# Performance work log

Measured on AMD Instinct MI355X. Metric: run time of the kernel, lower is better.

## Reference

```python
import jax, jax.numpy as jnp
import numpy as np

NUM_TYPES = 4
IN_DIM = 128
HID_DIM = 256
OUT_DIM = 128
NUM_NODES = 100000


def setup_inputs() -> dict:
    key = jax.random.key(0)
    k_x, k_t, k_w1, k_b1, k_w2, k_b2 = jax.random.split(key, 6)
    raw_features = jax.random.normal(k_x, (NUM_NODES, IN_DIM), dtype=jnp.float32)
    node_type = jax.random.randint(k_t, (NUM_NODES,), 0, NUM_TYPES, dtype=jnp.int64)
    # stacked per-type MLP params (Kaiming-ish scale like torch Linear defaults)
    W1 = jax.random.uniform(k_w1, (NUM_TYPES, IN_DIM, HID_DIM), dtype=jnp.float32,
                            minval=-1.0, maxval=1.0) / np.sqrt(IN_DIM)
    b1 = jax.random.uniform(k_b1, (NUM_TYPES, HID_DIM), dtype=jnp.float32,
                            minval=-1.0, maxval=1.0) / np.sqrt(IN_DIM)
    W2 = jax.random.uniform(k_w2, (NUM_TYPES, HID_DIM, OUT_DIM), dtype=jnp.float32,
                            minval=-1.0, maxval=1.0) / np.sqrt(HID_DIM)
    b2 = jax.random.uniform(k_b2, (NUM_TYPES, OUT_DIM), dtype=jnp.float32,
                            minval=-1.0, maxval=1.0) / np.sqrt(HID_DIM)
    return {"raw_features": raw_features, "node_type": node_type,
            "W1": W1, "b1": b1, "W2": W2, "b2": b2}


def reference(raw_features, node_type, W1, b1, W2, b2):
    # Run every expert on every node (num_types is tiny), then select per node.
    # h: [types, nodes, hidden]
    h = jax.nn.relu(jnp.einsum('ni,tih->tnh', raw_features, W1) + b1[:, None, :])
    # out_all: [types, nodes, out]
    out_all = jnp.einsum('tnh,tho->tno', h, W2) + b2[:, None, :]
    # select expert output matching each node's type -> [nodes, out]
    encoded = out_all[node_type, jnp.arange(raw_features.shape[0])]
    return encoded
```

## Files before the change

kernel.cpp:

```cpp
#include <hip/hip_runtime.h>
#include <hip/hip_bf16.h>

typedef float f32x4 __attribute__((ext_vector_type(4)));
typedef short short8 __attribute__((ext_vector_type(8)));

#define NTYPES 4


static __device__ __forceinline__ unsigned short f2bf(float f) {
  union { float f; unsigned int u; } v; v.f = f;
  unsigned int u = v.u;
  unsigned int r = u + 0x7FFFu + ((u >> 16) & 1u);
  return (unsigned short)(r >> 16);
}

static __device__ __forceinline__ unsigned int pkbf(float a, float b) {
  __hip_bfloat162 h = __float22bfloat162_rn(make_float2(a, b));
  union { __hip_bfloat162 h; unsigned int u; } v; v.h = h;
  return v.u;
}

#define LBAR() do { \
  __builtin_amdgcn_sched_barrier(0); \
  asm volatile("s_waitcnt lgkmcnt(0)" ::: "memory"); \
  __builtin_amdgcn_s_barrier(); \
  __builtin_amdgcn_sched_barrier(0); } while (0)

static __device__ __forceinline__ void prep_tile(int role, int tid,
    const float* __restrict__ W1, const float* __restrict__ W2,
    unsigned short* __restrict__ W1T, unsigned short* __restrict__ W2T,
    unsigned short (*sp)[72]) {
  const int bb = role & 31;
  const int tt = bb >> 3, ti = bb & 7;
  const float* src; unsigned short* dst; int scols, tr, tc;
  if (role < 32) { src = W1 + tt * 32768; dst = W1T + tt * 32768; scols = 256; tr = ti >> 2; tc = ti & 3; }
  else           { src = W2 + tt * 32768; dst = W2T + tt * 32768; scols = 128; tr = ti >> 1; tc = ti & 1; }
  const int srows = 32768 / scols;
  const int r0 = tid >> 4, cw = (tid & 15) << 2;
  #pragma unroll
  for (int i = 0; i < 4; ++i) {
    int r = tr * 64 + i * 16 + r0;
    float4 v = *(const float4*)(src + r * scols + tc * 64 + cw);
    sp[i * 16 + r0][cw + 0] = f2bf(v.x);
    sp[i * 16 + r0][cw + 1] = f2bf(v.y);
    sp[i * 16 + r0][cw + 2] = f2bf(v.z);
    sp[i * 16 + r0][cw + 3] = f2bf(v.w);
  }
  __syncthreads();
  #pragma unroll
  for (int i = 0; i < 4; ++i) {
    int orow = i * 16 + r0;
    ushort4 u;
    u.x = sp[cw + 0][orow];
    u.y = sp[cw + 1][orow];
    u.z = sp[cw + 2][orow];
    u.w = sp[cw + 3][orow];
    *(ushort4*)(dst + (tc * 64 + orow) * srows + tr * 64 + cw) = u;
  }
}

static __device__ __forceinline__ void mlp_body(
    int t, int lb, int nblk, int g0, int g1, int tid,
    const float* __restrict__ X, const int* __restrict__ perm,
    const unsigned short* __restrict__ W1T, const unsigned short* __restrict__ W2T,
    const float* __restrict__ B1, const float* __restrict__ B2,
    float* __restrict__ OUT, float* __restrict__ dump,
    unsigned char* x_lds, unsigned char* h_lds, int (*s_rid)[64]) {
  const int l  = tid & 63, w = tid >> 6;
  const int lo = l & 15,  hi = l >> 4;
  const int nt2 = g1 - g0 - lb;
  if (nt2 <= 0) return;
  const int cnt = (nt2 + nblk - 1) / nblk;

  const int rg = tid >> 5;
  const int c4 = (tid & 31) * 4;

  if (tid < 64) s_rid[0][tid] = perm[(g0 + lb) * 64 + tid];
  __syncthreads();
  float4 xv[8];
  #pragma unroll
  for (int p = 0; p < 8; ++p) {
    int rd = s_rid[0][p * 8 + rg];
    xv[p] = make_float4(0.f, 0.f, 0.f, 0.f);
    if (rd >= 0) xv[p] = *(const float4*)(X + (size_t)rd * 128 + c4);
  }

  const unsigned short* w1t = W1T + (t << 15);
  const unsigned short* w2t = W2T + (t << 15);
  short8 a1[4][4];
  #pragma unroll
  for (int ks = 0; ks < 4; ++ks)
    #pragma unroll
    for (int m = 0; m < 4; ++m)
      a1[ks][m] = *(const short8*)(w1t + (w * 64 + m * 16 + lo) * 128 + ks * 32 + hi * 8);
  short8 a2[8][2];
  #pragma unroll
  for (int ks = 0; ks < 8; ++ks)
    #pragma unroll
    for (int mo = 0; mo < 2; ++mo)
      a2[ks][mo] = *(const short8*)(w2t + (w * 32 + mo * 16 + lo) * 256 + ks * 32 + hi * 8);
  f32x4 bb1[4], bb2[2];
  #pragma unroll
  for (int m = 0; m < 4; ++m)
    bb1[m] = *(const f32x4*)(B1 + t * 256 + w * 64 + m * 16 + hi * 4);
  #pragma unroll
  for (int mo = 0; mo < 2; ++mo)
    bb2[mo] = *(const f32x4*)(B2 + t * 128 + w * 32 + mo * 16 + hi * 4);

  for (int j = 0; j < cnt; ++j) {
    const int g = g0 + lb + j * nblk;
    const bool hn = (j + 1 < cnt);
    const int cur = j & 1, nxt = cur ^ 1;
    unsigned char* xb = x_lds + (j & 1) * 16384;

    #pragma unroll
    for (int p = 0; p < 8; ++p) {
      int row = p * 8 + rg;
      uint2 u;
      u.x = pkbf(xv[p].x, xv[p].y);
      u.y = pkbf(xv[p].z, xv[p].w);
      int byte = (row * 256 + c4 * 2) ^ ((row & 7) << 4);
      *(uint2*)(xb + byte) = u;
    }
    LBAR();

    if (hn && tid < 64) s_rid[nxt][tid] = perm[(g + nblk) * 64 + tid];

    f32x4 acc[4][4];
    #pragma unroll
    for (int m = 0; m < 4; ++m)
      #pragma unroll
      for (int n2 = 0; n2 < 4; ++n2) acc[m][n2] = (f32x4){0.f, 0.f, 0.f, 0.f};
    #pragma unroll
    for (int ks = 0; ks < 4; ++ks) {
      short8 b[4];
      #pragma unroll
      for (int n2 = 0; n2 < 4; ++n2) {
        int row = n2 * 16 + lo;
        int byte = (row * 256 + ks * 64 + hi * 16) ^ ((row & 7) << 4);
        b[n2] = *(const short8*)(xb + byte);
      }
      #pragma unroll
      for (int m = 0; m < 4; ++m)
        #pragma unroll
        for (int n2 = 0; n2 < 4; ++n2)
          acc[m][n2] = __builtin_amdgcn_mfma_f32_16x16x32_bf16(a1[ks][m], b[n2], acc[m][n2], 0, 0, 0);
    }

    #pragma unroll
    for (int m = 0; m < 4; ++m) {
      const int hw2 = w * 128 + m * 32 + hi * 8;
      #pragma unroll
      for (int n2 = 0; n2 < 4; ++n2) {
        int node = n2 * 16 + lo;
        uint2 hu;
        hu.x = pkbf(fmaxf(acc[m][n2][0] + bb1[m][0], 0.f),
                    fmaxf(acc[m][n2][1] + bb1[m][1], 0.f));
        hu.y = pkbf(fmaxf(acc[m][n2][2] + bb1[m][2], 0.f),
                    fmaxf(acc[m][n2][3] + bb1[m][3], 0.f));
        int byte = (node * 512 + hw2) ^ ((node & 7) << 4);
        *(uint2*)(h_lds + byte) = hu;
      }
    }
    LBAR();

    float4 nv[8];
    #pragma unroll
    for (int p = 0; p < 8; ++p) nv[p] = make_float4(0.f, 0.f, 0.f, 0.f);
    if (hn) {
      #pragma unroll
      for (int p = 0; p < 8; ++p) {
        int rd = s_rid[nxt][p * 8 + rg];
        if (rd >= 0) nv[p] = *(const float4*)(X + (size_t)rd * 128 + c4);
      }
    }

    f32x4 acc2[2][4];
    #pragma unroll
    for (int mo = 0; mo < 2; ++mo)
      #pragma unroll
      for (int n2 = 0; n2 < 4; ++n2) acc2[mo][n2] = (f32x4){0.f, 0.f, 0.f, 0.f};
    #pragma unroll
    for (int ks = 0; ks < 8; ++ks) {
      short8 b[4];
      #pragma unroll
      for (int n2 = 0; n2 < 4; ++n2) {
        int node = n2 * 16 + lo;
        int byte = (node * 512 + ks * 64 + hi * 16) ^ ((node & 7) << 4);
        b[n2] = *(const short8*)(h_lds + byte);
      }
      #pragma unroll
      for (int mo = 0; mo < 2; ++mo)
        #pragma unroll
        for (int n2 = 0; n2 < 4; ++n2)
          acc2[mo][n2] = __builtin_amdgcn_mfma_f32_16x16x32_bf16(a2[ks][mo], b[n2], acc2[mo][n2], 0, 0, 0);
    }
    __syncthreads();

    #pragma unroll
    for (int mo = 0; mo < 2; ++mo) {
      const int oc = w * 32 + mo * 16 + hi * 4;
      #pragma unroll
      for (int n2 = 0; n2 < 4; ++n2) {
        int node = n2 * 16 + lo;
        f32x4 o = acc2[mo][n2];
        o[0] += bb2[mo][0]; o[1] += bb2[mo][1];
        o[2] += bb2[mo][2]; o[3] += bb2[mo][3];
        int byte = (node * 512 + oc * 4) ^ ((node & 7) << 4);
        *(f32x4*)(h_lds + byte) = o;
      }
    }
    LBAR();

    #pragma unroll
    for (int p = 0; p < 8; ++p) {
      int row = p * 8 + rg;
      int rd = s_rid[cur][row];
      f32x4 v = *(const f32x4*)(h_lds + ((row * 512 + c4 * 4) ^ ((row & 7) << 4)));
      float* dst = (rd >= 0) ? (OUT + (size_t)rd * 128 + c4) : (dump + c4);
      *(f32x4*)dst = v;
    }

    #pragma unroll
    for (int p = 0; p < 8; ++p) xv[p] = nv[p];
  }
}

__global__ __launch_bounds__(256) void k_hp(
    const float* __restrict__ W1, const float* __restrict__ W2,
    unsigned short* __restrict__ W1T, unsigned short* __restrict__ W2T,
    const int* __restrict__ NT, int n, int* __restrict__ cnts) {
  __shared__ unsigned short sp[64][72];
  __shared__ int lc[NTYPES];
  const int tid = threadIdx.x;
  if (blockIdx.x < 64) {
    prep_tile(blockIdx.x, tid, W1, W2, W1T, W2T, sp);
  } else {
    int hb = blockIdx.x - 64;
    if (tid < NTYPES) lc[tid] = 0;
    __syncthreads();
    int i = hb * 256 + tid;
    if (i < n) atomicAdd(&lc[NT[i]], 1);
    __syncthreads();
    if (tid < NTYPES) cnts[hb * NTYPES + tid] = lc[tid];
  }
}

__global__ __launch_bounds__(256) void k_scatter2(
    const int* __restrict__ NT, int n, const int* __restrict__ cnts, int nbH,
    int* __restrict__ perm, int* __restrict__ bases) {
  __shared__ int s_tot[NTYPES], s_pre[NTYPES], lc[NTYPES];
  const int tid = threadIdx.x;
  const int bid = blockIdx.x;
  const int l = tid & 63, w = tid >> 6;
  {
    int tot = 0, pre = 0;
    for (int b = l; b < nbH; b += 64) {
      int c = cnts[b * NTYPES + w];
      tot += c;
      pre += (b < bid) ? c : 0;
    }
    #pragma unroll
    for (int off = 32; off; off >>= 1) {
      tot += __shfl_down(tot, off);
      pre += __shfl_down(pre, off);
    }
    if (l == 0) { s_tot[w] = tot; s_pre[w] = pre; }
  }
  __syncthreads();
  int sb[NTYPES + 1];
  sb[0] = 0;
  #pragma unroll
  for (int tau = 0; tau < NTYPES; ++tau)
    sb[tau + 1] = sb[tau] + ((s_tot[tau] + 63) & ~63);
  if (bid == 0 && tid <= NTYPES) bases[tid] = sb[tid];
  if (tid < NTYPES) lc[tid] = 0;
  __syncthreads();
  int i = bid * 256 + tid;
  if (i < n) {
    int tt = NT[i];
    int r = atomicAdd(&lc[tt], 1);
    perm[sb[tt] + s_pre[tt] + r] = i;
  }
  if (bid < NTYPES) {
    for (int p = sb[bid] + s_tot[bid] + tid; p < sb[bid + 1]; p += 256)
      perm[p] = -1;
  }
}

__global__ __launch_bounds__(256, 1) void k_mlpw_fb(
    const float* __restrict__ X, const int* __restrict__ perm,
    const int* __restrict__ bases,
    const unsigned short* __restrict__ W1T, const unsigned short* __restrict__ W2T,
    const float* __restrict__ B1, const float* __restrict__ B2,
    float* __restrict__ OUT, float* __restrict__ dump) {
  __shared__ __align__(16) unsigned char x_lds[2 * 16384];
  __shared__ __align__(16) unsigned char h_lds[32768];
  __shared__ int s_rid[2][64];
  const int t = blockIdx.x >> 7, lb = blockIdx.x & 127;
  mlp_body(t, lb, 128, bases[t] >> 6, bases[t + 1] >> 6, threadIdx.x,
           X, perm, W1T, W2T, B1, B2, OUT, dump, x_lds, h_lds, s_rid);
}

extern "C" void kernel_launch(void* const* d_in, const int* in_sizes, int n_in,
                              void* d_out, int out_size, void* d_ws, size_t ws_size,
                              hipStream_t stream) {
  const float* X  = (const float*)d_in[0];
  const int*   NT = (const int*)d_in[1];
  const float* W1 = (const float*)d_in[2];
  const float* B1 = (const float*)d_in[3];
  const float* W2 = (const float*)d_in[4];
  const float* B2 = (const float*)d_in[5];
  float* OUT = (float*)d_out;
  int n = in_sizes[1];

  char* ws = (char*)d_ws;
  float* dump = (float*)(ws + 512);
  int* bases = (int*)(ws + 2048);
  int* cnts = (int*)(ws + 4096);
  int* perm = (int*)(ws + 16384);
  unsigned short* W1T = (unsigned short*)(ws + 524288);
  unsigned short* W2T = (unsigned short*)(ws + 786432);

  const int nbH = (n + 255) / 256;
  k_hp<<<64 + nbH, 256, 0, stream>>>(W1, W2, W1T, W2T, NT, n, cnts);
  k_scatter2<<<nbH, 256, 0, stream>>>(NT, n, cnts, nbH, perm, bases);
  k_mlpw_fb<<<512, 256, 0, stream>>>(X, perm, bases, W1T, W2T, B1, B2, OUT, dump);
}
```

Baseline: 51.28 us.

## Software-pipeline MLP layers across tiles with double-buffered hidden LDS and direct stores

Rewrites the grouped MLP kernel so that layer 1 of tile j and layer 2 of tile j-1 run in the same iteration, using double-buffered hidden activations in LDS. This drops to one barrier per iteration. Output goes straight from the accumulators to global memory instead of being staged through LDS, and per-row ids are read into registers rather than shared memory. The grid is halved from 512 to 256 blocks, one per CU with 64 blocks per type, so each block handles more tiles. The changes aim to cut barrier stalls and LDS traffic, at the cost of uncoalesced 16-byte output stores, repeated perm loads, and 96KB of LDS per block.

```diff
diff --git a/kernel.cpp b/kernel.cpp
--- a/kernel.cpp
+++ b/kernel.cpp
@@ -59,31 +59,28 @@
   }
 }
 
-static __device__ __forceinline__ void mlp_body(
-    int t, int lb, int nblk, int g0, int g1, int tid,
+__global__ __launch_bounds__(256, 1) void k_mlpn(
     const float* __restrict__ X, const int* __restrict__ perm,
+    const int* __restrict__ bases,
     const unsigned short* __restrict__ W1T, const unsigned short* __restrict__ W2T,
     const float* __restrict__ B1, const float* __restrict__ B2,
-    float* __restrict__ OUT, float* __restrict__ dump,
-    unsigned char* x_lds, unsigned char* h_lds, int (*s_rid)[64]) {
+    float* __restrict__ OUT) {
+  __shared__ __align__(16) unsigned char x_lds[2 * 16384];
+  __shared__ __align__(16) unsigned char h_lds[2 * 32768];
+
+  const int tid = threadIdx.x;
+  const int t  = blockIdx.x >> 6;
+  const int lb = blockIdx.x & 63;
+  const int g0 = bases[t] >> 6;
+  const int g1 = bases[t + 1] >> 6;
+  const int nt2 = g1 - g0 - lb;
+  if (nt2 <= 0) return;
+  const int cnt = (nt2 + 63) >> 6;
+
   const int l  = tid & 63, w = tid >> 6;
   const int lo = l & 15,  hi = l >> 4;
-  const int nt2 = g1 - g0 - lb;
-  if (nt2 <= 0) return;
-  const int cnt = (nt2 + nblk - 1) / nblk;
-
   const int rg = tid >> 5;
   const int c4 = (tid & 31) * 4;
-
-  if (tid < 64) s_rid[0][tid] = perm[(g0 + lb) * 64 + tid];
-  __syncthreads();
-  float4 xv[8];
-  #pragma unroll
-  for (int p = 0; p < 8; ++p) {
-    int rd = s_rid[0][p * 8 + rg];
-    xv[p] = make_float4(0.f, 0.f, 0.f, 0.f);
-    if (rd >= 0) xv[p] = *(const float4*)(X + (size_t)rd * 128 + c4);
-  }
 
   const unsigned short* w1t = W1T + (t << 15);
   const unsigned short* w2t = W2T + (t << 15);
@@ -107,122 +104,136 @@
   for (int mo = 0; mo < 2; ++mo)
     bb2[mo] = *(const f32x4*)(B2 + t * 128 + w * 32 + mo * 16 + hi * 4);
 
-  for (int j = 0; j < cnt; ++j) {
-    const int g = g0 + lb + j * nblk;
-    const bool hn = (j + 1 < cnt);
-    const int cur = j & 1, nxt = cur ^ 1;
-    unsigned char* xb = x_lds + (j & 1) * 16384;
-
+  int rid_n[8];
+  float4 xv_n[8];
+  {
+    const int gg = (g0 + lb) * 64;
+    #pragma unroll
+    for (int p = 0; p < 8; ++p) rid_n[p] = perm[gg + p * 8 + rg];
+    #pragma unroll
+    for (int p = 0; p < 8; ++p) {
+      xv_n[p] = make_float4(0.f, 0.f, 0.f, 0.f);
+      if (rid_n[p] >= 0) xv_n[p] = *(const float4*)(X + (size_t)rid_n[p] * 128 + c4);
+    }
     #pragma unroll
     for (int p = 0; p < 8; ++p) {
       int row = p * 8 + rg;
       uint2 u;
-      u.x = pkbf(xv[p].x, xv[p].y);
-      u.y = pkbf(xv[p].z, xv[p].w);
-      int byte = (row * 256 + c4 * 2) ^ ((row & 7) << 4);
-      *(uint2*)(xb + byte) = u;
-    }
+      u.x = pkbf(xv_n[p].x, xv_n[p].y);
+      u.y = pkbf(xv_n[p].z, xv_n[p].w);
+      *(uint2*)(x_lds + ((row * 256 + c4 * 2) ^ ((row & 7) << 4))) = u;
+    }
+  }
+
+  for (int j = 0; j <= cnt; ++j) {
+    const int g = g0 + lb + j * 64;
+    const bool hn = (j + 1 < cnt);
+    const bool h1 = (j < cnt);
+    unsigned char* xb = x_lds + (j & 1) * 16384;
+    unsigned char* hb = h_lds + (j & 1) * 32768;
+    unsigned char* hp = h_lds + ((j & 1) ^ 1) * 32768;
+
     LBAR();
 
-    if (hn && tid < 64) s_rid[nxt][tid] = perm[(g + nblk) * 64 + tid];
-
-    f32x4 acc[4][4];
-    #pragma unroll
-    for (int m = 0; m < 4; ++m)
-      #pragma unroll
-      for (int n2 = 0; n2 < 4; ++n2) acc[m][n2] = (f32x4){0.f, 0.f, 0.f, 0.f};
-    #pragma unroll
-    for (int ks = 0; ks < 4; ++ks) {
-      short8 b[4];
-      #pragma unroll
-      for (int n2 = 0; n2 < 4; ++n2) {
-        int row = n2 * 16 + lo;
-        int byte = (row * 256 + ks * 64 + hi * 16) ^ ((row & 7) << 4);
-        b[n2] = *(const short8*)(xb + byte);
-      }
+    if (hn) {
+      const int gg = (g + 64) * 64;
+      #pragma unroll
+      for (int p = 0; p < 8; ++p) rid_n[p] = perm[gg + p * 8 + rg];
+      #pragma unroll
+      for (int p = 0; p < 8; ++p) {
+        xv_n[p] = make_float4(0.f, 0.f, 0.f, 0.f);
+        if (rid_n[p] >= 0) xv_n[p] = *(const float4*)(X + (size_t)rid_n[p] * 128 + c4);
+      }
+    }
+
+    if (h1) {
+      f32x4 acc[4][4];
       #pragma unroll
       for (int m = 0; m < 4; ++m)
         #pragma unroll
-        for (int n2 = 0; n2 < 4; ++n2)
-          acc[m][n2] = __builtin_amdgcn_mfma_f32_16x16x32_bf16(a1[ks][m], b[n2], acc[m][n2], 0, 0, 0);
-    }
-
-    #pragma unroll
-    for (int m = 0; m < 4; ++m) {
-      const int hw2 = w * 128 + m * 32 + hi * 8;
-      #pragma unroll
-      for (int n2 = 0; n2 < 4; ++n2) {
-        int node = n2 * 16 + lo;
-        uint2 hu;
-        hu.x = pkbf(fmaxf(acc[m][n2][0] + bb1[m][0], 0.f),
-                    fmaxf(acc[m][n2][1] + bb1[m][1], 0.f));
-        hu.y = pkbf(fmaxf(acc[m][n2][2] + bb1[m][2], 0.f),
-                    fmaxf(acc[m][n2][3] + bb1[m][3], 0.f));
-        int byte = (node * 512 + hw2) ^ ((node & 7) << 4);
-        *(uint2*)(h_lds + byte) = hu;
-      }
-    }
-    LBAR();
-
-    float4 nv[8];
-    #pragma unroll
-    for (int p = 0; p < 8; ++p) nv[p] = make_float4(0.f, 0.f, 0.f, 0.f);
+        for (int n2 = 0; n2 < 4; ++n2) acc[m][n2] = (f32x4){0.f, 0.f, 0.f, 0.f};
+      #pragma unroll
+      for (int ks = 0; ks < 4; ++ks) {
+        short8 b[4];
+        #pragma unroll
+        for (int n2 = 0; n2 < 4; ++n2) {
+          int row = n2 * 16 + lo;
+          int byte = (row * 256 + ks * 64 + hi * 16) ^ ((row & 7) << 4);
+          b[n2] = *(const short8*)(xb + byte);
+        }
+        #pragma unroll
+        for (int m = 0; m < 4; ++m)
+          #pragma unroll
+          for (int n2 = 0; n2 < 4; ++n2)
+            acc[m][n2] = __builtin_amdgcn_mfma_f32_16x16x32_bf16(a1[ks][m], b[n2], acc[m][n2], 0, 0, 0);
+      }
+      #pragma unroll
+      for (int m = 0; m < 4; ++m) {
+        const int hw2 = w * 128 + m * 32 + hi * 8;
+        #pragma unroll
+        for (int n2 = 0; n2 < 4; ++n2) {
+          int node = n2 * 16 + lo;
+          uint2 hu;
+          hu.x = pkbf(fmaxf(acc[m][n2][0] + bb1[m][0], 0.f),
+                      fmaxf(acc[m][n2][1] + bb1[m][1], 0.f));
+          hu.y = pkbf(fmaxf(acc[m][n2][2] + bb1[m][2], 0.f),
+                      fmaxf(acc[m][n2][3] + bb1[m][3], 0.f));
+          int byte = (node * 512 + hw2) ^ ((node & 7) << 4);
+          *(uint2*)(hb + byte) = hu;
+        }
+      }
+    }
+
+    if (j > 0) {
+      f32x4 acc2[2][4];
+      #pragma unroll
+      for (int mo = 0; mo < 2; ++mo)
+        #pragma unroll
+        for (int n2 = 0; n2 < 4; ++n2) acc2[mo][n2] = (f32x4){0.f, 0.f, 0.f, 0.f};
+      #pragma unroll
+      for (int ks = 0; ks < 8; ++ks) {
+        short8 b[4];
+        #pragma unroll
+        for (int n2 = 0; n2 < 4; ++n2) {
+          int node = n2 * 16 + lo;
+          int byte = (node * 512 + ks * 64 + hi * 16) ^ ((node & 7) << 4);
+          b[n2] = *(const short8*)(hp + byte);
+        }
+        #pragma unroll
+        for (int mo = 0; mo < 2; ++mo)
+          #pragma unroll
+          for (int n2 = 0; n2 < 4; ++n2)
+            acc2[mo][n2] = __builtin_amdgcn_mfma_f32_16x16x32_bf16(a2[ks][mo], b[n2], acc2[mo][n2], 0, 0, 0);
+      }
+      const int gp = (g - 64) * 64;
+      #pragma unroll
+      for (int mo = 0; mo < 2; ++mo) {
+        const int oc = w * 32 + mo * 16 + hi * 4;
+        #pragma unroll
+        for (int n2 = 0; n2 < 4; ++n2) {
+          int row = n2 * 16 + lo;
+          int rd = perm[gp + row];
+          if (rd >= 0) {
+            f32x4 o = acc2[mo][n2];
+            o[0] += bb2[mo][0]; o[1] += bb2[mo][1];
+            o[2] += bb2[mo][2]; o[3] += bb2[mo][3];
+            *(f32x4*)(OUT + (size_t)rd * 128 + oc) = o;
+          }
+        }
+      }
+    }
+
     if (hn) {
+      unsigned char* xn = x_lds + ((j & 1) ^ 1) * 16384;
       #pragma unroll
       for (int p = 0; p < 8; ++p) {
-        int rd = s_rid[nxt][p * 8 + rg];
-        if (rd >= 0) nv[p] = *(const float4*)(X + (size_t)rd * 128 + c4);
-      }
-    }
-
-    f32x4 acc2[2][4];
-    #pragma unroll
-    for (int mo = 0; mo < 2; ++mo)
-      #pragma unroll
-      for (int n2 = 0; n2 < 4; ++n2) acc2[mo][n2] = (f32x4){0.f, 0.f, 0.f, 0.f};
-    #pragma unroll
-    for (int ks = 0; ks < 8; ++ks) {
-      short8 b[4];
-      #pragma unroll
-      for (int n2 = 0; n2 < 4; ++n2) {
-        int node = n2 * 16 + lo;
-        int byte = (node * 512 + ks * 64 + hi * 16) ^ ((node & 7) << 4);
-        b[n2] = *(const short8*)(h_lds + byte);
-      }
-      #pragma unroll
-      for (int mo = 0; mo < 2; ++mo)
-        #pragma unroll
-        for (int n2 = 0; n2 < 4; ++n2)
-          acc2[mo][n2] = __builtin_amdgcn_mfma_f32_16x16x32_bf16(a2[ks][mo], b[n2], acc2[mo][n2], 0, 0, 0);
-    }
-    __syncthreads();
-
-    #pragma unroll
-    for (int mo = 0; mo < 2; ++mo) {
-      const int oc = w * 32 + mo * 16 + hi * 4;
-      #pragma unroll
-      for (int n2 = 0; n2 < 4; ++n2) {
-        int node = n2 * 16 + lo;
-        f32x4 o = acc2[mo][n2];
-        o[0] += bb2[mo][0]; o[1] += bb2[mo][1];
-        o[2] += bb2[mo][2]; o[3] += bb2[mo][3];
-        int byte = (node * 512 + oc * 4) ^ ((node & 7) << 4);
-        *(f32x4*)(h_lds + byte) = o;
-      }
-    }
-    LBAR();
-
-    #pragma unroll
-    for (int p = 0; p < 8; ++p) {
-      int row = p * 8 + rg;
-      int rd = s_rid[cur][row];
-      f32x4 v = *(const f32x4*)(h_lds + ((row * 512 + c4 * 4) ^ ((row & 7) << 4)));
-      float* dst = (rd >= 0) ? (OUT + (size_t)rd * 128 + c4) : (dump + c4);
-      *(f32x4*)dst = v;
-    }
-
-    #pragma unroll
-    for (int p = 0; p < 8; ++p) xv[p] = nv[p];
+        int row = p * 8 + rg;
+        uint2 u;
+        u.x = pkbf(xv_n[p].x, xv_n[p].y);
+        u.y = pkbf(xv_n[p].z, xv_n[p].w);
+        *(uint2*)(xn + ((row * 256 + c4 * 2) ^ ((row & 7) << 4))) = u;
+      }
+    }
   }
 }
 
@@ -288,20 +299,6 @@
   }
 }
 
-__global__ __launch_bounds__(256, 1) void k_mlpw_fb(
-    const float* __restrict__ X, const int* __restrict__ perm,
-    const int* __restrict__ bases,
-    const unsigned short* __restrict__ W1T, const unsigned short* __restrict__ W2T,
-    const float* __restrict__ B1, const float* __restrict__ B2,
-    float* __restrict__ OUT, float* __restrict__ dump) {
-  __shared__ __align__(16) unsigned char x_lds[2 * 16384];
-  __shared__ __align__(16) unsigned char h_lds[32768];
-  __shared__ int s_rid[2][64];
-  const int t = blockIdx.x >> 7, lb = blockIdx.x & 127;
-  mlp_body(t, lb, 128, bases[t] >> 6, bases[t + 1] >> 6, threadIdx.x,
-           X, perm, W1T, W2T, B1, B2, OUT, dump, x_lds, h_lds, s_rid);
-}
-
 extern "C" void kernel_launch(void* const* d_in, const int* in_sizes, int n_in,
                               void* d_out, int out_size, void* d_ws, size_t ws_size,
                               hipStream_t stream) {
@@ -315,7 +312,6 @@
   int n = in_sizes[1];
 
   char* ws = (char*)d_ws;
-  float* dump = (float*)(ws + 512);
   int* bases = (int*)(ws + 2048);
   int* cnts = (int*)(ws + 4096);
   int* perm = (int*)(ws + 16384);
@@ -325,5 +321,5 @@
   const int nbH = (n + 255) / 256;
   k_hp<<<64 + nbH, 256, 0, stream>>>(W1, W2, W1T, W2T, NT, n, cnts);
   k_scatter2<<<nbH, 256, 0, stream>>>(NT, n, cnts, nbH, perm, bases);
-  k_mlpw_fb<<<512, 256, 0, stream>>>(X, perm, bases, W1T, W2T, B1, B2, OUT, dump);
-}
+  k_mlpn<<<256, 256, 0, stream>>>(X, perm, bases, W1T, W2T, B1, B2, OUT);
+}
```

Result: slower. 61.85 us (+20.6%).
